# Performance work log

Measured on AMD Instinct MI355X. Metric: run time of the kernel, lower is better.

The kernel has to match this reference:

```python
import jax, jax.numpy as jnp
import numpy as np

N_NODES = 50000


def sage_conv(x, src, dst, W_l, b_l, W_r, n_nodes):
    """PyG SAGEConv with mean aggregation: lin_l(mean_{j->i} x_j) + lin_r(x_i)."""
    msg = x[src]                                            # [E, d]
    agg = jax.ops.segment_sum(msg, dst, num_segments=n_nodes)
    cnt = jax.ops.segment_sum(jnp.ones((src.shape[0],), x.dtype), dst,
                              num_segments=n_nodes)
    agg = agg / jnp.maximum(cnt, 1.0)[:, None]              # mean over in-neighbors
    return agg @ W_l.T + b_l + x @ W_r.T


def setup_inputs() -> dict:
    key = jax.random.key(0)
    ks = jax.random.split(key, 8)
    d_in, d_hid, d_out = 128, 128, 64
    E = 600000
    x = jax.random.normal(ks[0], (N_NODES, d_in), dtype=jnp.float32)
    edge_index = jax.random.randint(ks[1], (2, E), 0, N_NODES, dtype=jnp.int64)
    s = 1.0 / np.sqrt(d_in)
    return {
        "x": x,
        "edge_index": edge_index,
        "W1_l": jax.random.normal(ks[2], (d_hid, d_in), jnp.float32) * s,
        "b1": jnp.zeros((d_hid,), jnp.float32),
        "W1_r": jax.random.normal(ks[3], (d_hid, d_in), jnp.float32) * s,
        "W2_l": jax.random.normal(ks[4], (d_out, d_hid), jnp.float32) * s,
        "b2": jnp.zeros((d_out,), jnp.float32),
        "W2_r": jax.random.normal(ks[5], (d_out, d_hid), jnp.float32) * s,
    }


def reference(x, edge_index, W1_l, b1, W1_r, W2_l, b2, W2_r):
    src, dst = edge_index[0], edge_index[1]
    h = sage_conv(x, src, dst, W1_l, b1, W1_r, N_NODES)
    h = jax.nn.relu(h)
    h = sage_conv(h, src, dst, W2_l, b2, W2_r, N_NODES)
    return jax.nn.log_softmax(h, axis=1)
```

## Files before the change

kernel.cpp:

```cpp
#include <hip/hip_runtime.h>
#include <math.h>

#define N_NODES 50000
#define D 128
#define D_OUT 64

typedef short bf16x8 __attribute__((ext_vector_type(8)));
typedef float f32x4  __attribute__((ext_vector_type(4)));
typedef unsigned short u16x8 __attribute__((ext_vector_type(8)));

__device__ __forceinline__ unsigned short f_to_bf16(float f) {
    unsigned int u = __float_as_uint(f);
    u = (u + 0x7fffu + ((u >> 16) & 1u)) >> 16;
    return (unsigned short)u;
}
__device__ __forceinline__ float bf16lo(unsigned int v) { return __uint_as_float(v << 16); }
__device__ __forceinline__ float bf16hi(unsigned int v) { return __uint_as_float(v & 0xffff0000u); }
__device__ __forceinline__ float bf16f(unsigned short v) { return __uint_as_float((unsigned int)v << 16); }

__device__ __forceinline__ void conv8(const float* __restrict__ src, unsigned short* __restrict__ dst, int i)
{
    float4 v0 = *reinterpret_cast<const float4*>(src + i);
    float4 v1 = *reinterpret_cast<const float4*>(src + i + 4);
    u16x8 o;
    o[0] = f_to_bf16(v0.x); o[1] = f_to_bf16(v0.y);
    o[2] = f_to_bf16(v0.z); o[3] = f_to_bf16(v0.w);
    o[4] = f_to_bf16(v1.x); o[5] = f_to_bf16(v1.y);
    o[6] = f_to_bf16(v1.z); o[7] = f_to_bf16(v1.w);
    *reinterpret_cast<u16x8*>(dst + i) = o;
}

__device__ __forceinline__ void acc_add(float* acc, uint4 v)
{
    acc[0] += bf16lo(v.x); acc[1] += bf16hi(v.x);
    acc[2] += bf16lo(v.y); acc[3] += bf16hi(v.y);
    acc[4] += bf16lo(v.z); acc[5] += bf16hi(v.z);
    acc[6] += bf16lo(v.w); acc[7] += bf16hi(v.w);
}

__global__ __launch_bounds__(256) void zero_kernel(int* __restrict__ p, int n4)
{
    int i = blockIdx.x * 256 + threadIdx.x;
    if (i < n4) *reinterpret_cast<int4*>(p + i * 4) = make_int4(0, 0, 0, 0);
}

__global__ __launch_bounds__(256) void prep_kernel(
    const float* __restrict__ x, unsigned short* __restrict__ xb,
    const float* __restrict__ w1l, const float* __restrict__ w1r,
    const float* __restrict__ w2l, const float* __restrict__ w2r,
    unsigned short* __restrict__ Wb,
    const int* __restrict__ dst, int* __restrict__ deg,
    int XB, int E)
{
    const int bx = blockIdx.x;
    if (bx < XB) {
        int i = (bx * 256 + threadIdx.x) * 8;
        if (i < N_NODES * D) conv8(x, xb, i);
    } else if (bx < XB + 24) {
        int i = ((bx - XB) * 256 + threadIdx.x) * 8;
        const float* src; int off;
        if      (i < 16384) { src = w1l; off = 0; }
        else if (i < 32768) { src = w1r; off = 16384; }
        else if (i < 40960) { src = w2l; off = 32768; }
        else                { src = w2r; off = 40960; }
        conv8(src, Wb + off, i - off);
    } else {
        int e = (bx - XB - 24) * 256 + threadIdx.x;
        if (e < E) atomicAdd(&deg[dst[e]], 1);
    }
}

__global__ __launch_bounds__(256) void scan1_kernel(
    const int* __restrict__ deg, int* __restrict__ part,
    int* __restrict__ bsum, int n)
{
    const int t = threadIdx.x;
    const int base = blockIdx.x * 1024 + t * 4;

    int a0 = 0, a1 = 0, a2 = 0, a3 = 0;
    if (base + 3 < n) {
        int4 v = *reinterpret_cast<const int4*>(deg + base);
        a0 = v.x; a1 = v.y; a2 = v.z; a3 = v.w;
    } else if (base < n) {
        a0 = deg[base];
        if (base + 1 < n) a1 = deg[base + 1];
        if (base + 2 < n) a2 = deg[base + 2];
    }
    const int s0 = a0, s1 = s0 + a1, s2 = s1 + a2, s3 = s2 + a3;

    const int lane = t & 63;
    int incl = s3;
#pragma unroll
    for (int off = 1; off < 64; off <<= 1) {
        int up = __shfl_up(incl, off);
        if (lane >= off) incl += up;
    }

    __shared__ int wsum[4];
    const int wid = t >> 6;
    if (lane == 63) wsum[wid] = incl;
    __syncthreads();

    int woff = 0;
#pragma unroll
    for (int w = 0; w < 4; ++w) woff += (w < wid) ? wsum[w] : 0;

    const int ex = woff + incl - s3;
    if (base + 3 < n) {
        int4 o; o.x = ex; o.y = ex + s0; o.z = ex + s1; o.w = ex + s2;
        *reinterpret_cast<int4*>(part + base) = o;
    } else if (base < n) {
        part[base] = ex;
        if (base + 1 < n) part[base + 1] = ex + s0;
        if (base + 2 < n) part[base + 2] = ex + s1;
    }
    if (t == 255) bsum[blockIdx.x] = woff + incl;
}

__global__ __launch_bounds__(256) void scan3_kernel(
    const int* __restrict__ part, const int* __restrict__ bsum,
    int* __restrict__ row_ptr, int nb, int n)
{
    __shared__ int sAdd, sTot;
    const int t = threadIdx.x;
    const int bid = blockIdx.x;

    if (t < 64) {
        int v   = (t < nb) ? bsum[t] : 0;
        int add = (t < bid) ? v : 0;
        int tot = v;
#pragma unroll
        for (int off = 1; off < 64; off <<= 1) {
            add += __shfl_xor(add, off);
            tot += __shfl_xor(tot, off);
        }
        if (t == 0) { sAdd = add; sTot = tot; }
    }
    __syncthreads();

    const int add = sAdd;
    const int base = bid * 1024 + t * 4;
    if (base + 3 < n) {
        int4 v = *reinterpret_cast<const int4*>(part + base);
        v.x += add; v.y += add; v.z += add; v.w += add;
        *reinterpret_cast<int4*>(row_ptr + base) = v;
    } else if (base < n) {
        row_ptr[base] = part[base] + add;
        if (base + 1 < n) row_ptr[base + 1] = part[base + 1] + add;
        if (base + 2 < n) row_ptr[base + 2] = part[base + 2] + add;
    }
    if (bid == nb - 1 && t == 0) row_ptr[n] = sTot;
}

__global__ __launch_bounds__(256) void fill_kernel(
    const int* __restrict__ src, const int* __restrict__ dst,
    const int* __restrict__ row_ptr, int* __restrict__ cursor,
    int* __restrict__ esrc, int E)
{
    int e = blockIdx.x * blockDim.x + threadIdx.x;
    if (e >= E) return;
    int d = dst[e];
    int pos = atomicAdd(&cursor[d], 1);
    esrc[row_ptr[d] + pos] = src[e];
}

template<int CHUNKS>
__global__ __launch_bounds__(256) void gather_bf16_kernel(
    const unsigned short* __restrict__ xb,
    const int* __restrict__ row_ptr,
    const int* __restrict__ esrc,
    unsigned short* __restrict__ aggb,
    int n_nodes)
{
    constexpr int RPL = 64 / CHUNKS;
    constexpr int NLOADS = 8;
    constexpr int ITER = RPL * NLOADS;
    const int wv   = threadIdx.x >> 6;
    const int lane = threadIdx.x & 63;
    const int node = blockIdx.x * 4 + wv;
    if (node >= n_nodes) return;

    const int beg = row_ptr[node];
    const int end = row_ptr[node + 1];
    const int g = lane / CHUNKS;
    const int c = lane % CHUNKS;

    const uint4* x4 = reinterpret_cast<const uint4*>(xb);

    float acc[8];
#pragma unroll
    for (int k = 0; k < 8; ++k) acc[k] = 0.f;

    for (int base = beg; base < end; base += 64) {
        const int cnt = min(end - base, 64);
        int s = (base + lane < end) ? esrc[base + lane] : 0;
        for (int i = 0; i < cnt; i += ITER) {
            int pp[NLOADS]; uint4 vv[NLOADS]; bool ok[NLOADS];
#pragma unroll
            for (int j = 0; j < NLOADS; ++j) {
                pp[j] = i + j * RPL + g;
                int sj = __shfl(s, pp[j] & 63);
                ok[j] = pp[j] < cnt;
                if (ok[j]) vv[j] = x4[(size_t)sj * CHUNKS + c];
            }
#pragma unroll
            for (int j = 0; j < NLOADS; ++j)
                if (ok[j]) acc_add(acc, vv[j]);
        }
    }

#pragma unroll
    for (int k = 0; k < 8; ++k) {
#pragma unroll
        for (int off = CHUNKS; off < 64; off <<= 1)
            acc[k] += __shfl_xor(acc[k], off);
    }

    if (g == 0) {
        const float inv = (end > beg) ? 1.0f / (float)(end - beg) : 0.0f;
        uint4 o;
        o.x = (unsigned int)f_to_bf16(acc[0] * inv) | ((unsigned int)f_to_bf16(acc[1] * inv) << 16);
        o.y = (unsigned int)f_to_bf16(acc[2] * inv) | ((unsigned int)f_to_bf16(acc[3] * inv) << 16);
        o.z = (unsigned int)f_to_bf16(acc[4] * inv) | ((unsigned int)f_to_bf16(acc[5] * inv) << 16);
        o.w = (unsigned int)f_to_bf16(acc[6] * inv) | ((unsigned int)f_to_bf16(acc[7] * inv) << 16);
        reinterpret_cast<uint4*>(aggb)[(size_t)node * CHUNKS + c] = o;
    }
}

__global__ __launch_bounds__(256) void layer1_mfma_kernel(
    const unsigned short* __restrict__ aggb,
    const unsigned short* __restrict__ xb,
    const unsigned short* __restrict__ Wb,
    const float* __restrict__ b1,
    unsigned short* __restrict__ h1b,
    unsigned short* __restrict__ t2b,
    int n_tiles)
{
    __shared__ unsigned short As[64][136];
    __shared__ unsigned short Xs[64][136];
    __shared__ unsigned short Hs[64][136];

    const int tid  = threadIdx.x;
    const int wv   = tid >> 6, lane = tid & 63;
    const int tile0 = blockIdx.x * 4;
    const int node0 = tile0 * 16;

    for (int q = tid; q < 1024; q += 256) {
        const int row = q >> 4, c = q & 15;
        const int node = node0 + row;
        uint4 va = make_uint4(0, 0, 0, 0), vx = va;
        if (node < N_NODES) {
            va = reinterpret_cast<const uint4*>(aggb)[(size_t)node * 16 + c];
            vx = reinterpret_cast<const uint4*>(xb)  [(size_t)node * 16 + c];
        }
        *reinterpret_cast<uint4*>(&As[row][c * 8]) = va;
        *reinterpret_cast<uint4*>(&Xs[row][c * 8]) = vx;
    }
    __syncthreads();

    const int c16 = lane & 15, kg = lane >> 4;

#pragma unroll
    for (int jj = 0; jj < 2; ++jj) {
        const int jt = wv + jj * 4;
        bf16x8 wlf[4], wrf[4];
        {
            const unsigned short* wl = Wb +         (size_t)(jt * 16 + c16) * D + kg * 8;
            const unsigned short* wr = Wb + 16384 + (size_t)(jt * 16 + c16) * D + kg * 8;
#pragma unroll
            for (int kf = 0; kf < 4; ++kf) {
                wlf[kf] = *reinterpret_cast<const bf16x8*>(wl + kf * 32);
                wrf[kf] = *reinterpret_cast<const bf16x8*>(wr + kf * 32);
            }
        }
        const float bias = b1[jt * 16 + c16];

#pragma unroll
        for (int t = 0; t < 4; ++t) {
            if (tile0 + t < n_tiles) {
                const int r0 = t * 16;
                f32x4 acc = {0.f, 0.f, 0.f, 0.f};
#pragma unroll
                for (int kf = 0; kf < 4; ++kf) {
                    bf16x8 a0 = *reinterpret_cast<const bf16x8*>(&As[r0 + c16][kg * 8 + kf * 32]);
                    acc = __builtin_amdgcn_mfma_f32_16x16x32_bf16(a0, wlf[kf], acc, 0, 0, 0);
                }
#pragma unroll
                for (int kf = 0; kf < 4; ++kf) {
                    bf16x8 a1 = *reinterpret_cast<const bf16x8*>(&Xs[r0 + c16][kg * 8 + kf * 32]);
                    acc = __builtin_amdgcn_mfma_f32_16x16x32_bf16(a1, wrf[kf], acc, 0, 0, 0);
                }
#pragma unroll
                for (int i = 0; i < 4; ++i) {
                    const int row = r0 + kg * 4 + i;
                    float v = fmaxf(acc[i] + bias, 0.0f);
                    unsigned short us = f_to_bf16(v);
                    h1b[(size_t)(node0 + row) * D + jt * 16 + c16] = us;
                    Hs[row][jt * 16 + c16] = us;
                }
            }
        }
    }
    __syncthreads();

    {
        const int jt = wv;
        bf16x8 w2f[4];
        {
            const unsigned short* wl = Wb + 32768 + (size_t)(jt * 16 + c16) * D + kg * 8;
#pragma unroll
            for (int kf = 0; kf < 4; ++kf)
                w2f[kf] = *reinterpret_cast<const bf16x8*>(wl + kf * 32);
        }
#pragma unroll
        for (int t = 0; t < 4; ++t) {
            if (tile0 + t < n_tiles) {
                const int r0 = t * 16;
                f32x4 acc = {0.f, 0.f, 0.f, 0.f};
#pragma unroll
                for (int kf = 0; kf < 4; ++kf) {
                    bf16x8 a2 = *reinterpret_cast<const bf16x8*>(&Hs[r0 + c16][kg * 8 + kf * 32]);
                    acc = __builtin_amdgcn_mfma_f32_16x16x32_bf16(a2, w2f[kf], acc, 0, 0, 0);
                }
#pragma unroll
                for (int i = 0; i < 4; ++i)
                    t2b[(size_t)(node0 + r0 + kg * 4 + i) * D_OUT + jt * 16 + c16] = f_to_bf16(acc[i]);
            }
        }
    }
}

__global__ __launch_bounds__(256) void layer2_mfma_kernel(
    const unsigned short* __restrict__ agg2b,
    const unsigned short* __restrict__ h1b,
    const unsigned short* __restrict__ Wb,
    const float* __restrict__ b2,
    float* __restrict__ out,
    int n_tiles)
{
    __shared__ float zs[64][68];

    const int tid  = threadIdx.x;
    const int wv   = tid >> 6, lane = tid & 63;
    const int tile0 = blockIdx.x * 4;
    const int node0 = tile0 * 16;
    const int c16 = lane & 15, kg = lane >> 4;

    const int jt = wv;
    bf16x8 wf[4];
    {
        const unsigned short* wr = Wb + 40960 + (size_t)(jt * 16 + c16) * D + kg * 8;
#pragma unroll
        for (int kf = 0; kf < 4; ++kf)
            wf[kf] = *reinterpret_cast<const bf16x8*>(wr + kf * 32);
    }
    const float bias = b2[jt * 16 + c16];

#pragma unroll
    for (int t = 0; t < 4; ++t) {
        if (tile0 + t < n_tiles) {
            const int r0 = t * 16;
            f32x4 acc = {0.f, 0.f, 0.f, 0.f};
            const unsigned short* A1 = h1b + (size_t)(node0 + r0 + c16) * D + kg * 8;
#pragma unroll
            for (int kf = 0; kf < 4; ++kf) {
                bf16x8 a = *reinterpret_cast<const bf16x8*>(A1 + kf * 32);
                acc = __builtin_amdgcn_mfma_f32_16x16x32_bf16(a, wf[kf], acc, 0, 0, 0);
            }
#pragma unroll
            for (int i = 0; i < 4; ++i) {
                const int row = r0 + kg * 4 + i;
                float lft = bf16f(agg2b[(size_t)(node0 + row) * D_OUT + jt * 16 + c16]);
                zs[row][jt * 16 + c16] = lft + acc[i] + bias;
            }
        }
    }
    __syncthreads();

    for (int r = 0; r < 16; ++r) {
        const int row = wv * 16 + r;
        if (tile0 + (row >> 4) >= n_tiles) break;
        float z = zs[row][lane];
        float m = z;
#pragma unroll
        for (int off = 1; off < 64; off <<= 1)
            m = fmaxf(m, __shfl_xor(m, off));
        float e = expf(z - m);
        float s = e;
#pragma unroll
        for (int off = 1; off < 64; off <<= 1)
            s += __shfl_xor(s, off);
        out[(size_t)(node0 + row) * D_OUT + lane] = z - m - logf(s);
    }
}

extern "C" void kernel_launch(void* const* d_in, const int* in_sizes, int n_in,
                              void* d_out, int out_size, void* d_ws, size_t ws_size,
                              hipStream_t stream)
{
    const float* x   = (const float*)d_in[0];
    const int*   ei  = (const int*)d_in[1];
    const float* W1l = (const float*)d_in[2];
    const float* b1  = (const float*)d_in[3];
    const float* W1r = (const float*)d_in[4];
    const float* W2l = (const float*)d_in[5];
    const float* b2  = (const float*)d_in[6];
    const float* W2r = (const float*)d_in[7];
    float* out = (float*)d_out;

    const int E = in_sizes[1] / 2;
    const int* src = ei;
    const int* dst = ei + E;

    char* base = (char*)d_ws;
    size_t off = 0;
    auto take = [&](size_t bytes) { char* p = base + off; off += (bytes + 255) & ~(size_t)255; return p; };

    unsigned short* xb    = (unsigned short*)take((size_t)N_NODES * D * 2);
    unsigned short* aggb  = (unsigned short*)take((size_t)N_NODES * D * 2);
    unsigned short* h1b   = (unsigned short*)take((size_t)N_NODES * D * 2);
    unsigned short* t2b   = (unsigned short*)take((size_t)N_NODES * D_OUT * 2);
    unsigned short* agg2b = (unsigned short*)take((size_t)N_NODES * D_OUT * 2);
    unsigned short* Wb    = (unsigned short*)take((size_t)49152 * 2);
    int* degcur  = (int*)take((size_t)2 * N_NODES * 4);
    int* deg     = degcur;
    int* cursor  = degcur + N_NODES;
    int* row_ptr = (int*)take(((size_t)N_NODES + 1) * 4);
    int* part    = (int*)take((size_t)N_NODES * 4);
    int* bsum    = (int*)take((size_t)64 * 4);
    int* esrc    = (int*)take((size_t)E * 4);

    const int EB = (E + 255) / 256;
    const int SB = (N_NODES + 1023) / 1024;
    const int XB = (N_NODES * D / 8 + 255) / 256;
    const int GB = (N_NODES + 3) / 4;
    const int NT = N_NODES / 16;
    const int LB = (NT + 3) / 4;

    zero_kernel<<<(2 * N_NODES / 4 + 255) / 256, 256, 0, stream>>>(degcur, 2 * N_NODES / 4);
    prep_kernel<<<XB + 24 + EB, 256, 0, stream>>>(x, xb, W1l, W1r, W2l, W2r, Wb, dst, deg, XB, E);
    scan1_kernel<<<SB, 256, 0, stream>>>(deg, part, bsum, N_NODES);
    scan3_kernel<<<SB, 256, 0, stream>>>(part, bsum, row_ptr, SB, N_NODES);
    fill_kernel<<<EB, 256, 0, stream>>>(src, dst, row_ptr, cursor, esrc, E);

    gather_bf16_kernel<16><<<GB, 256, 0, stream>>>(xb, row_ptr, esrc, aggb, N_NODES);
    layer1_mfma_kernel<<<LB, 256, 0, stream>>>(aggb, xb, Wb, b1, h1b, t2b, NT);

    gather_bf16_kernel<8><<<GB, 256, 0, stream>>>(t2b, row_ptr, esrc, agg2b, N_NODES);
    layer2_mfma_kernel<<<LB, 256, 0, stream>>>(agg2b, h1b, Wb, b2, out, NT);
}
```

Measured before the change: 161.1 us.

## Fuse layer-2 root matmul into layer1 and softmax into second gather

Layer1 now computes both the left (W2_l) and right (W2_r) projections of layer 2, writing bf16 t2b and an fp32 r2 with the bias folded in. The h1 buffer is no longer written out, and the separate layer2 kernel is removed. The second gather adds r2 and does log_softmax in-register, and the CSR fill seeds the cursor with row_ptr so the extra row_ptr read goes away. This saves one kernel launch and the h1/agg2 round trips, but adds a 12.8MB fp32 r2 write and read.

```diff
diff --git a/kernel.cpp b/kernel.cpp
--- a/kernel.cpp
+++ b/kernel.cpp
@@ -16,7 +16,6 @@
 }
 __device__ __forceinline__ float bf16lo(unsigned int v) { return __uint_as_float(v << 16); }
 __device__ __forceinline__ float bf16hi(unsigned int v) { return __uint_as_float(v & 0xffff0000u); }
-__device__ __forceinline__ float bf16f(unsigned short v) { return __uint_as_float((unsigned int)v << 16); }
 
 __device__ __forceinline__ void conv8(const float* __restrict__ src, unsigned short* __restrict__ dst, int i)
 {
@@ -119,7 +118,7 @@
 
 __global__ __launch_bounds__(256) void scan3_kernel(
     const int* __restrict__ part, const int* __restrict__ bsum,
-    int* __restrict__ row_ptr, int nb, int n)
+    int* __restrict__ row_ptr, int* __restrict__ cursor, int nb, int n)
 {
     __shared__ int sAdd, sTot;
     const int t = threadIdx.x;
@@ -144,27 +143,27 @@
         int4 v = *reinterpret_cast<const int4*>(part + base);
         v.x += add; v.y += add; v.z += add; v.w += add;
         *reinterpret_cast<int4*>(row_ptr + base) = v;
+        *reinterpret_cast<int4*>(cursor + base)  = v;
     } else if (base < n) {
-        row_ptr[base] = part[base] + add;
-        if (base + 1 < n) row_ptr[base + 1] = part[base + 1] + add;
-        if (base + 2 < n) row_ptr[base + 2] = part[base + 2] + add;
+        for (int q = 0; q < 3 && base + q < n; ++q) {
+            int v = part[base + q] + add;
+            row_ptr[base + q] = v;
+            cursor[base + q]  = v;
+        }
     }
     if (bid == nb - 1 && t == 0) row_ptr[n] = sTot;
 }
 
 __global__ __launch_bounds__(256) void fill_kernel(
     const int* __restrict__ src, const int* __restrict__ dst,
-    const int* __restrict__ row_ptr, int* __restrict__ cursor,
-    int* __restrict__ esrc, int E)
+    int* __restrict__ cursor, int* __restrict__ esrc, int E)
 {
     int e = blockIdx.x * blockDim.x + threadIdx.x;
     if (e >= E) return;
-    int d = dst[e];
-    int pos = atomicAdd(&cursor[d], 1);
-    esrc[row_ptr[d] + pos] = src[e];
-}
-
-template<int CHUNKS>
+    int pos = atomicAdd(&cursor[dst[e]], 1);
+    esrc[pos] = src[e];
+}
+
 __global__ __launch_bounds__(256) void gather_bf16_kernel(
     const unsigned short* __restrict__ xb,
     const int* __restrict__ row_ptr,
@@ -172,6 +171,7 @@
     unsigned short* __restrict__ aggb,
     int n_nodes)
 {
+    constexpr int CHUNKS = 16;
     constexpr int RPL = 64 / CHUNKS;
     constexpr int NLOADS = 8;
     constexpr int ITER = RPL * NLOADS;
@@ -211,9 +211,8 @@
 
 #pragma unroll
     for (int k = 0; k < 8; ++k) {
-#pragma unroll
-        for (int off = CHUNKS; off < 64; off <<= 1)
-            acc[k] += __shfl_xor(acc[k], off);
+        acc[k] += __shfl_xor(acc[k], 16);
+        acc[k] += __shfl_xor(acc[k], 32);
     }
 
     if (g == 0) {
@@ -232,8 +231,9 @@
     const unsigned short* __restrict__ xb,
     const unsigned short* __restrict__ Wb,
     const float* __restrict__ b1,
-    unsigned short* __restrict__ h1b,
+    const float* __restrict__ b2,
     unsigned short* __restrict__ t2b,
+    float* __restrict__ r2,
     int n_tiles)
 {
     __shared__ unsigned short As[64][136];
@@ -294,9 +294,7 @@
                 for (int i = 0; i < 4; ++i) {
                     const int row = r0 + kg * 4 + i;
                     float v = fmaxf(acc[i] + bias, 0.0f);
-                    unsigned short us = f_to_bf16(v);
-                    h1b[(size_t)(node0 + row) * D + jt * 16 + c16] = us;
-                    Hs[row][jt * 16 + c16] = us;
+                    Hs[row][jt * 16 + c16] = f_to_bf16(v);
                 }
             }
         }
@@ -305,92 +303,128 @@
 
     {
         const int jt = wv;
-        bf16x8 w2f[4];
+        bf16x8 w2l[4], w2r[4];
         {
             const unsigned short* wl = Wb + 32768 + (size_t)(jt * 16 + c16) * D + kg * 8;
-#pragma unroll
-            for (int kf = 0; kf < 4; ++kf)
-                w2f[kf] = *reinterpret_cast<const bf16x8*>(wl + kf * 32);
-        }
+            const unsigned short* wr = Wb + 40960 + (size_t)(jt * 16 + c16) * D + kg * 8;
+#pragma unroll
+            for (int kf = 0; kf < 4; ++kf) {
+                w2l[kf] = *reinterpret_cast<const bf16x8*>(wl + kf * 32);
+                w2r[kf] = *reinterpret_cast<const bf16x8*>(wr + kf * 32);
+            }
+        }
+        const float bias2 = b2[jt * 16 + c16];
+
 #pragma unroll
         for (int t = 0; t < 4; ++t) {
             if (tile0 + t < n_tiles) {
                 const int r0 = t * 16;
-                f32x4 acc = {0.f, 0.f, 0.f, 0.f};
+                bf16x8 af[4];
+#pragma unroll
+                for (int kf = 0; kf < 4; ++kf)
+                    af[kf] = *reinterpret_cast<const bf16x8*>(&Hs[r0 + c16][kg * 8 + kf * 32]);
+
+                f32x4 accT = {0.f, 0.f, 0.f, 0.f};
+                f32x4 accR = {0.f, 0.f, 0.f, 0.f};
 #pragma unroll
                 for (int kf = 0; kf < 4; ++kf) {
-                    bf16x8 a2 = *reinterpret_cast<const bf16x8*>(&Hs[r0 + c16][kg * 8 + kf * 32]);
-                    acc = __builtin_amdgcn_mfma_f32_16x16x32_bf16(a2, w2f[kf], acc, 0, 0, 0);
+                    accT = __builtin_amdgcn_mfma_f32_16x16x32_bf16(af[kf], w2l[kf], accT, 0, 0, 0);
+                    accR = __builtin_amdgcn_mfma_f32_16x16x32_bf16(af[kf], w2r[kf], accR, 0, 0, 0);
                 }
 #pragma unroll
-                for (int i = 0; i < 4; ++i)
-                    t2b[(size_t)(node0 + r0 + kg * 4 + i) * D_OUT + jt * 16 + c16] = f_to_bf16(acc[i]);
-            }
-        }
-    }
-}
-
-__global__ __launch_bounds__(256) void layer2_mfma_kernel(
-    const unsigned short* __restrict__ agg2b,
-    const unsigned short* __restrict__ h1b,
-    const unsigned short* __restrict__ Wb,
-    const float* __restrict__ b2,
+                for (int i = 0; i < 4; ++i) {
+                    const int node = node0 + r0 + kg * 4 + i;
+                    t2b[(size_t)node * D_OUT + jt * 16 + c16] = f_to_bf16(accT[i]);
+                    r2 [(size_t)node * D_OUT + jt * 16 + c16] = accR[i] + bias2;
+                }
+            }
+        }
+    }
+}
+
+__global__ __launch_bounds__(256) void gather2_sm_kernel(
+    const unsigned short* __restrict__ t2b,
+    const float* __restrict__ r2,
+    const int* __restrict__ row_ptr,
+    const int* __restrict__ esrc,
     float* __restrict__ out,
-    int n_tiles)
-{
-    __shared__ float zs[64][68];
-
-    const int tid  = threadIdx.x;
-    const int wv   = tid >> 6, lane = tid & 63;
-    const int tile0 = blockIdx.x * 4;
-    const int node0 = tile0 * 16;
-    const int c16 = lane & 15, kg = lane >> 4;
-
-    const int jt = wv;
-    bf16x8 wf[4];
-    {
-        const unsigned short* wr = Wb + 40960 + (size_t)(jt * 16 + c16) * D + kg * 8;
-#pragma unroll
-        for (int kf = 0; kf < 4; ++kf)
-            wf[kf] = *reinterpret_cast<const bf16x8*>(wr + kf * 32);
-    }
-    const float bias = b2[jt * 16 + c16];
-
-#pragma unroll
-    for (int t = 0; t < 4; ++t) {
-        if (tile0 + t < n_tiles) {
-            const int r0 = t * 16;
-            f32x4 acc = {0.f, 0.f, 0.f, 0.f};
-            const unsigned short* A1 = h1b + (size_t)(node0 + r0 + c16) * D + kg * 8;
-#pragma unroll
-            for (int kf = 0; kf < 4; ++kf) {
-                bf16x8 a = *reinterpret_cast<const bf16x8*>(A1 + kf * 32);
-                acc = __builtin_amdgcn_mfma_f32_16x16x32_bf16(a, wf[kf], acc, 0, 0, 0);
-            }
-#pragma unroll
-            for (int i = 0; i < 4; ++i) {
-                const int row = r0 + kg * 4 + i;
-                float lft = bf16f(agg2b[(size_t)(node0 + row) * D_OUT + jt * 16 + c16]);
-                zs[row][jt * 16 + c16] = lft + acc[i] + bias;
-            }
-        }
-    }
-    __syncthreads();
-
-    for (int r = 0; r < 16; ++r) {
-        const int row = wv * 16 + r;
-        if (tile0 + (row >> 4) >= n_tiles) break;
-        float z = zs[row][lane];
-        float m = z;
-#pragma unroll
-        for (int off = 1; off < 64; off <<= 1)
-            m = fmaxf(m, __shfl_xor(m, off));
-        float e = expf(z - m);
-        float s = e;
-#pragma unroll
-        for (int off = 1; off < 64; off <<= 1)
-            s += __shfl_xor(s, off);
-        out[(size_t)(node0 + row) * D_OUT + lane] = z - m - logf(s);
+    int n_nodes)
+{
+    constexpr int CHUNKS = 8;
+    constexpr int RPL = 64 / CHUNKS;
+    constexpr int NLOADS = 8;
+    constexpr int ITER = RPL * NLOADS;
+    const int wv   = threadIdx.x >> 6;
+    const int lane = threadIdx.x & 63;
+    const int node = blockIdx.x * 4 + wv;
+    if (node >= n_nodes) return;
+
+    const int beg = row_ptr[node];
+    const int end = row_ptr[node + 1];
+    const int g = lane / CHUNKS;
+    const int c = lane % CHUNKS;
+
+    const uint4* t4 = reinterpret_cast<const uint4*>(t2b);
+
+    float acc[8];
+#pragma unroll
+    for (int k = 0; k < 8; ++k) acc[k] = 0.f;
+
+    for (int base = beg; base < end; base += 64) {
+        const int cnt = min(end - base, 64);
+        int s = (base + lane < end) ? esrc[base + lane] : 0;
+        for (int i = 0; i < cnt; i += ITER) {
+            int pp[NLOADS]; uint4 vv[NLOADS]; bool ok[NLOADS];
+#pragma unroll
+            for (int j = 0; j < NLOADS; ++j) {
+                pp[j] = i + j * RPL + g;
+                int sj = __shfl(s, pp[j] & 63);
+                ok[j] = pp[j] < cnt;
+                if (ok[j]) vv[j] = t4[(size_t)sj * CHUNKS + c];
+            }
+#pragma unroll
+            for (int j = 0; j < NLOADS; ++j)
+                if (ok[j]) acc_add(acc, vv[j]);
+        }
+    }
+
+#pragma unroll
+    for (int k = 0; k < 8; ++k) {
+        acc[k] += __shfl_xor(acc[k], 8);
+        acc[k] += __shfl_xor(acc[k], 16);
+        acc[k] += __shfl_xor(acc[k], 32);
+    }
+
+    const float inv = (end > beg) ? 1.0f / (float)(end - beg) : 0.0f;
+
+    float4 ra = *reinterpret_cast<const float4*>(r2 + (size_t)node * D_OUT + c * 8);
+    float4 rb = *reinterpret_cast<const float4*>(r2 + (size_t)node * D_OUT + c * 8 + 4);
+    float z[8];
+    z[0] = acc[0] * inv + ra.x; z[1] = acc[1] * inv + ra.y;
+    z[2] = acc[2] * inv + ra.z; z[3] = acc[3] * inv + ra.w;
+    z[4] = acc[4] * inv + rb.x; z[5] = acc[5] * inv + rb.y;
+    z[6] = acc[6] * inv + rb.z; z[7] = acc[7] * inv + rb.w;
+
+    float m = z[0];
+#pragma unroll
+    for (int k = 1; k < 8; ++k) m = fmaxf(m, z[k]);
+#pragma unroll
+    for (int off = 1; off < 8; off <<= 1)
+        m = fmaxf(m, __shfl_xor(m, off));
+    float s = 0.f;
+#pragma unroll
+    for (int k = 0; k < 8; ++k) s += expf(z[k] - m);
+#pragma unroll
+    for (int off = 1; off < 8; off <<= 1)
+        s += __shfl_xor(s, off);
+    const float lse = m + logf(s);
+
+    if (g == 0) {
+        float4 oa, ob;
+        oa.x = z[0] - lse; oa.y = z[1] - lse; oa.z = z[2] - lse; oa.w = z[3] - lse;
+        ob.x = z[4] - lse; ob.y = z[5] - lse; ob.z = z[6] - lse; ob.w = z[7] - lse;
+        *reinterpret_cast<float4*>(out + (size_t)node * D_OUT + c * 8)     = oa;
+        *reinterpret_cast<float4*>(out + (size_t)node * D_OUT + c * 8 + 4) = ob;
     }
 }
 
@@ -416,15 +450,13 @@
     size_t off = 0;
     auto take = [&](size_t bytes) { char* p = base + off; off += (bytes + 255) & ~(size_t)255; return p; };
 
-    unsigned short* xb    = (unsigned short*)take((size_t)N_NODES * D * 2);
-    unsigned short* aggb  = (unsigned short*)take((size_t)N_NODES * D * 2);
-    unsigned short* h1b   = (unsigned short*)take((size_t)N_NODES * D * 2);
-    unsigned short* t2b   = (unsigned short*)take((size_t)N_NODES * D_OUT * 2);
-    unsigned short* agg2b = (unsigned short*)take((size_t)N_NODES * D_OUT * 2);
-    unsigned short* Wb    = (unsigned short*)take((size_t)49152 * 2);
-    int* degcur  = (int*)take((size_t)2 * N_NODES * 4);
-    int* deg     = degcur;
-    int* cursor  = degcur + N_NODES;
+    unsigned short* xb   = (unsigned short*)take((size_t)N_NODES * D * 2);
+    unsigned short* aggb = (unsigned short*)take((size_t)N_NODES * D * 2);
+    unsigned short* t2b  = (unsigned short*)take((size_t)N_NODES * D_OUT * 2);
+    float*          r2   = (float*)         take((size_t)N_NODES * D_OUT * 4);
+    unsigned short* Wb   = (unsigned short*)take((size_t)49152 * 2);
+    int* deg     = (int*)take((size_t)N_NODES * 4);
+    int* cursor  = (int*)take((size_t)N_NODES * 4);
     int* row_ptr = (int*)take(((size_t)N_NODES + 1) * 4);
     int* part    = (int*)take((size_t)N_NODES * 4);
     int* bsum    = (int*)take((size_t)64 * 4);
@@ -437,15 +469,14 @@
     const int NT = N_NODES / 16;
     const int LB = (NT + 3) / 4;
 
-    zero_kernel<<<(2 * N_NODES / 4 + 255) / 256, 256, 0, stream>>>(degcur, 2 * N_NODES / 4);
+    zero_kernel<<<(N_NODES / 4 + 255) / 256, 256, 0, stream>>>(deg, N_NODES / 4);
     prep_kernel<<<XB + 24 + EB, 256, 0, stream>>>(x, xb, W1l, W1r, W2l, W2r, Wb, dst, deg, XB, E);
     scan1_kernel<<<SB, 256, 0, stream>>>(deg, part, bsum, N_NODES);
-    scan3_kernel<<<SB, 256, 0, stream>>>(part, bsum, row_ptr, SB, N_NODES);
-    fill_kernel<<<EB, 256, 0, stream>>>(src, dst, row_ptr, cursor, esrc, E);
-
-    gather_bf16_kernel<16><<<GB, 256, 0, stream>>>(xb, row_ptr, esrc, aggb, N_NODES);
-    layer1_mfma_kernel<<<LB, 256, 0, stream>>>(aggb, xb, Wb, b1, h1b, t2b, NT);
-
-    gather_bf16_kernel<8><<<GB, 256, 0, stream>>>(t2b, row_ptr, esrc, agg2b, N_NODES);
-    layer2_mfma_kernel<<<LB, 256, 0, stream>>>(agg2b, h1b, Wb, b2, out, NT);
-}
+    scan3_kernel<<<SB, 256, 0, stream>>>(part, bsum, row_ptr, cursor, SB, N_NODES);
+    fill_kernel<<<EB, 256, 0, stream>>>(src, dst, cursor, esrc, E);
+
+    gather_bf16_kernel<<<GB, 256, 0, stream>>>(xb, row_ptr, esrc, aggb, N_NODES);
+    layer1_mfma_kernel<<<LB, 256, 0, stream>>>(aggb, xb, Wb, b1, b2, t2b, r2, NT);
+
+    gather2_sm_kernel<<<GB, 256, 0, stream>>>(t2b, r2, row_ptr, esrc, out, N_NODES);
+}
```

After: 149.3 us. -7.3%, faster.
